# Kernel tuning notes

Measured on AMD Instinct MI355X. Metric: run time of the kernel, lower is better.

The kernel has to match this reference:

```python
import jax, jax.numpy as jnp
import numpy as np

N = 20000        # nodes
E = 640000       # edges (avg degree 32)
IN, H1, H2 = 512, 256, 128

def setup_inputs() -> dict:
    key = jax.random.key(0)
    k_feat, k_ew, k_src, k_dst, k_w1, k_w2 = jax.random.split(key, 6)
    return {
        "features": jax.random.normal(k_feat, (N, IN), jnp.float32),
        "edge_weight": jax.random.uniform(k_ew, (E,), jnp.float32),
        "src": jax.random.randint(k_src, (E,), 0, N),
        "dst": jax.random.randint(k_dst, (E,), 0, N),
        # learned params (GraphConv weight uses xavier-style init; bias zeros)
        "W1": jax.random.normal(k_w1, (IN, H1), jnp.float32) / np.float32(np.sqrt(IN)),
        "b1": jnp.zeros((H1,), jnp.float32),
        "W2": jax.random.normal(k_w2, (H1, H2), jnp.float32) / np.float32(np.sqrt(H1)),
        "b2": jnp.zeros((H2,), jnp.float32),
    }

def reference(features, edge_weight, src, dst, W1, b1, W2, b2):
    seg = lambda v, idx: jax.ops.segment_sum(v, idx, num_segments=N)

    # --- EdgeWeightNorm(norm='both'):
    # w_e / sqrt(out_wsum(src_e) * in_wsum(dst_e))
    out_wsum = seg(edge_weight, src)           # weighted out-degree  [N]
    in_wsum = seg(edge_weight, dst)            # weighted in-degree   [N]
    nw = edge_weight * jax.lax.rsqrt(out_wsum[src]) * jax.lax.rsqrt(in_wsum[dst])  # [E]

    # --- GraphConv layer 1: norm='none', edge_weight=nw, relu
    # in_feats > out_feats -> transform first, then weighted aggregation
    h = features @ W1                          # [N, H1]
    h = seg(h[src] * nw[:, None], dst) + b1    # SpMM: sum_e nw_e * h[src_e] at dst
    h = jax.nn.relu(h)

    # --- GraphConv layer 2: norm='both' (plain degrees, clamped min 1), identity act
    ones_e = jnp.ones((E,), h.dtype)
    out_deg = jnp.maximum(seg(ones_e, src), 1.0)   # out-degrees [N]
    in_deg = jnp.maximum(seg(ones_e, dst), 1.0)    # in-degrees  [N]
    h = h * jax.lax.rsqrt(out_deg)[:, None]        # src-side norm
    h = h @ W2                                     # [N, H2] (in > out -> W first)
    h = seg(h[src], dst)                           # unweighted sum aggregation
    h = h * jax.lax.rsqrt(in_deg)[:, None] + b2    # dst-side norm + bias
    return h
```

## Files before the change

kernel.cpp:

```cpp
#include <hip/hip_runtime.h>
#include <hip/hip_bf16.h>
#include <hip/hip_fp16.h>
#include <stdint.h>

#define IN_F 512
#define H1_F 256
#define H2_F 128
#define MPAD 20096
#define NN   20000
#define NPAIR 10000
#define BH   128
#define CAP  128
#define GB1  (157 * 2)

typedef __attribute__((ext_vector_type(8))) _Float16 half8;
typedef __attribute__((ext_vector_type(4))) float f32x4;
typedef __attribute__((ext_vector_type(4))) uint32_t u32x4;

__device__ inline __half2 h2cast(uint32_t v) { return __builtin_bit_cast(__half2, v); }
__device__ inline uint32_t h2bits(__half2 v) { return __builtin_bit_cast(uint32_t, v); }

__device__ inline void gld_lds16(const uint32_t* g, uint32_t* l) {
    __builtin_amdgcn_global_load_lds((const __attribute__((address_space(1))) uint32_t*)g,
                                     (__attribute__((address_space(3))) uint32_t*)l,
                                     16, 0, 0);
}

__global__ __launch_bounds__(512) void build_and_pack(
        const int* __restrict__ dst, const int* __restrict__ src,
        const float* __restrict__ ew,
        uint32_t* __restrict__ Pd, uint32_t* __restrict__ Ps, int E, int CH,
        const float4* __restrict__ X, ushort4* __restrict__ P, int n4,
        const float* __restrict__ W1, const float* __restrict__ W2,
        uint16_t* __restrict__ Bt1, uint16_t* __restrict__ Bt2) {
    __shared__ uint32_t pd[NN];
    __shared__ uint32_t ps[NN];
    const int b = blockIdx.x, tid = threadIdx.x;
    if (b < BH) {
        for (int i = tid; i < NN; i += 512) { pd[i] = 0; ps[i] = 0; }
        __syncthreads();
        const int e0 = b * CH, e1 = min(e0 + CH, E);
        for (int e = e0 + tid; e < e1; e += 512) {
            uint32_t v = (1u << 24) | (uint32_t)__float2uint_rn(ew[e] * 65536.0f);
            atomicAdd(&pd[dst[e]], v);
            atomicAdd(&ps[src[e]], v);
        }
        __syncthreads();
        for (int i = tid; i < NN; i += 512) {
            Pd[(size_t)b * NN + i] = pd[i];
            Ps[(size_t)b * NN + i] = ps[i];
        }
    } else {
        const int pbid = b - BH;
        const int PBLK = gridDim.x - BH;
        const int stride = PBLK * 512;
        const int t1 = IN_F * H1_F;
        const int total = n4 + t1 + H1_F * H2_F;
        for (int idx = pbid * 512 + tid; idx < total; idx += stride) {
            if (idx < n4) {
                float4 x = X[idx];
                ushort4 o;
                o.x = __builtin_bit_cast(unsigned short, (_Float16)x.x);
                o.y = __builtin_bit_cast(unsigned short, (_Float16)x.y);
                o.z = __builtin_bit_cast(unsigned short, (_Float16)x.z);
                o.w = __builtin_bit_cast(unsigned short, (_Float16)x.w);
                P[idx] = o;
            } else {
                int i = idx - n4;
                if (i < t1) {
                    int k = i / H1_F, n = i - k * H1_F;
                    Bt1[(size_t)n * IN_F + k] =
                        __builtin_bit_cast(unsigned short, (_Float16)W1[i]);
                } else {
                    int i2 = i - t1;
                    int k = i2 / H2_F, n = i2 - k * H2_F;
                    Bt2[(size_t)n * H1_F + k] =
                        __builtin_bit_cast(unsigned short, (_Float16)W2[i2]);
                }
            }
        }
    }
}

__global__ __launch_bounds__(256, 1) void gemm1_and_offsets(
        const uint16_t* __restrict__ At, const uint16_t* __restrict__ Bt,
        __half* __restrict__ Cout, int M, int K,
        const uint32_t* __restrict__ Pd, const uint32_t* __restrict__ Ps,
        uint16_t* __restrict__ Od,
        int* __restrict__ in_cnt, int* __restrict__ out_cnt,
        float* __restrict__ in_rs, float* __restrict__ out_rs, int N) {
    __shared__ uint32_t Al[128 * 16];
    __shared__ uint32_t Bl[128 * 16];
    const int bx = blockIdx.x;
    const int tid = threadIdx.x;
    if (bx >= GB1) {
        int i = (bx - GB1) * 256 + tid;
        if (i >= N) return;
        uint32_t cin = 0, cout = 0, win = 0, wout = 0;
        for (int b = 0; b < BH; ++b) {
            uint32_t vd = Pd[(size_t)b * NN + i];
            Od[(size_t)b * NN + i] = (uint16_t)cin;
            cin += vd >> 24; win += vd & 0xFFFFFFu;
            uint32_t vs = Ps[(size_t)b * NN + i];
            cout += vs >> 24; wout += vs & 0xFFFFFFu;
        }
        in_cnt[i] = (int)cin;
        out_cnt[i] = (int)cout;
        in_rs[i]  = cin  ? rsqrtf((float)win  * (1.0f / 65536.0f)) : 0.f;
        out_rs[i] = cout ? rsqrtf((float)wout * (1.0f / 65536.0f)) : 0.f;
        return;
    }
    const int xg = bx % 157, yg = bx / 157;
    const int lane = tid & 63, wid = tid >> 6;
    const int wm = wid >> 1, wn = wid & 1;
    const int l15 = lane & 15, lhi = lane >> 4;
    const int brow = xg * 128, bcol = yg * 128;

    f32x4 acc[4][4];
#pragma unroll
    for (int m = 0; m < 4; ++m)
#pragma unroll
        for (int n = 0; n < 4; ++n) acc[m][n] = f32x4{0.f, 0.f, 0.f, 0.f};

    for (int k0 = 0; k0 < K; k0 += 32) {
#pragma unroll
        for (int i = 0; i < 2; ++i) {
            int chunk = i * 256 + tid;
            int r = chunk >> 2, c16 = chunk & 3;
            int c16s = c16 ^ ((r & 3) ^ ((r >> 2) & 3));
            gld_lds16((const uint32_t*)(At + (size_t)(brow + r) * K + k0) + c16s * 4,
                      Al + chunk * 4);
        }
#pragma unroll
        for (int i = 0; i < 2; ++i) {
            int chunk = i * 256 + tid;
            int r = chunk >> 2, c16 = chunk & 3;
            int c16s = c16 ^ ((r & 3) ^ ((r >> 2) & 3));
            gld_lds16((const uint32_t*)(Bt + (size_t)(bcol + r) * K + k0) + c16s * 4,
                      Bl + chunk * 4);
        }
        __syncthreads();

        half8 am[4], bm[4];
#pragma unroll
        for (int m = 0; m < 4; ++m) {
            int row = wm * 64 + m * 16 + l15;
            int sA = (row & 3) ^ ((row >> 2) & 3);
            am[m] = __builtin_bit_cast(half8,
                        *(const u32x4*)(Al + row * 16 + ((lhi ^ sA) << 2)));
        }
#pragma unroll
        for (int n = 0; n < 4; ++n) {
            int col = wn * 64 + n * 16 + l15;
            int sB = (col & 3) ^ ((col >> 2) & 3);
            bm[n] = __builtin_bit_cast(half8,
                        *(const u32x4*)(Bl + col * 16 + ((lhi ^ sB) << 2)));
        }

#pragma unroll
        for (int m = 0; m < 4; ++m)
#pragma unroll
            for (int n = 0; n < 4; ++n)
                acc[m][n] = __builtin_amdgcn_mfma_f32_16x16x32_f16(am[m], bm[n],
                                                                   acc[m][n], 0, 0, 0);
        __syncthreads();
    }

#pragma unroll
    for (int m = 0; m < 4; ++m) {
        int rbase = brow + wm * 64 + m * 16 + lhi * 4;
#pragma unroll
        for (int n = 0; n < 4; ++n) {
            int col = bcol + wn * 64 + n * 16 + l15;
#pragma unroll
            for (int j = 0; j < 4; ++j) {
                int row = rbase + j;
                if (row < M)
                    Cout[(size_t)row * H1_F + col] = __float2half(acc[m][n][j]);
            }
        }
    }
}

__global__ __launch_bounds__(512) void scatter_dst(
        const int* __restrict__ src, const int* __restrict__ dst,
        const float* __restrict__ ew,
        const uint16_t* __restrict__ Od,
        const float* __restrict__ in_rs, const float* __restrict__ out_rs,
        unsigned long long* __restrict__ s_pk, int E, int CH) {
    __shared__ uint32_t h[NPAIR];
    const int b = blockIdx.x, tid = threadIdx.x;
    for (int i = tid; i < NPAIR; i += 512) h[i] = 0;
    __syncthreads();
    const int e0 = b * CH, e1 = min(e0 + CH, E);
    const uint16_t* Ob = Od + (size_t)b * NN;
    for (int e = e0 + tid; e < e1; e += 512) {
        int d = dst[e];
        uint32_t old = atomicAdd(&h[d >> 1], 1u << ((d & 1) * 16));
        uint32_t rank = (old >> ((d & 1) * 16)) & 0xffffu;
        int s = src[e];
        float nw = ew[e] * out_rs[s] * in_rs[d];
        int p = d * CAP + (int)Ob[d] + (int)rank;
        s_pk[p] = (unsigned long long)(unsigned)s |
                  ((unsigned long long)__builtin_bit_cast(unsigned, nw) << 32);
    }
}

__global__ __launch_bounds__(256, 1) void gemm2_f16(
        const uint16_t* __restrict__ At, const uint16_t* __restrict__ Bt,
        __half* __restrict__ Cout, const int* __restrict__ rowcnt,
        int M, int Nout, int K) {
    __shared__ uint32_t Al[128 * 16];
    __shared__ uint32_t Bl[128 * 16];
    const int tid = threadIdx.x;
    const int lane = tid & 63, wid = tid >> 6;
    const int wm = wid >> 1, wn = wid & 1;
    const int l15 = lane & 15, lhi = lane >> 4;
    const int brow = blockIdx.x * 128, bcol = blockIdx.y * 128;

    f32x4 acc[4][4];
#pragma unroll
    for (int m = 0; m < 4; ++m)
#pragma unroll
        for (int n = 0; n < 4; ++n) acc[m][n] = f32x4{0.f, 0.f, 0.f, 0.f};

    for (int k0 = 0; k0 < K; k0 += 32) {
#pragma unroll
        for (int i = 0; i < 2; ++i) {
            int chunk = i * 256 + tid;
            int r = chunk >> 2, c16 = chunk & 3;
            int c16s = c16 ^ ((r & 3) ^ ((r >> 2) & 3));
            gld_lds16((const uint32_t*)(At + (size_t)(brow + r) * K + k0) + c16s * 4,
                      Al + chunk * 4);
        }
#pragma unroll
        for (int i = 0; i < 2; ++i) {
            int chunk = i * 256 + tid;
            int r = chunk >> 2, c16 = chunk & 3;
            int c16s = c16 ^ ((r & 3) ^ ((r >> 2) & 3));
            gld_lds16((const uint32_t*)(Bt + (size_t)(bcol + r) * K + k0) + c16s * 4,
                      Bl + chunk * 4);
        }
        __syncthreads();

        half8 am[4], bm[4];
#pragma unroll
        for (int m = 0; m < 4; ++m) {
            int row = wm * 64 + m * 16 + l15;
            int sA = (row & 3) ^ ((row >> 2) & 3);
            am[m] = __builtin_bit_cast(half8,
                        *(const u32x4*)(Al + row * 16 + ((lhi ^ sA) << 2)));
        }
#pragma unroll
        for (int n = 0; n < 4; ++n) {
            int col = wn * 64 + n * 16 + l15;
            int sB = (col & 3) ^ ((col >> 2) & 3);
            bm[n] = __builtin_bit_cast(half8,
                        *(const u32x4*)(Bl + col * 16 + ((lhi ^ sB) << 2)));
        }

#pragma unroll
        for (int m = 0; m < 4; ++m)
#pragma unroll
            for (int n = 0; n < 4; ++n)
                acc[m][n] = __builtin_amdgcn_mfma_f32_16x16x32_f16(am[m], bm[n],
                                                                   acc[m][n], 0, 0, 0);
        __syncthreads();
    }

#pragma unroll
    for (int m = 0; m < 4; ++m) {
        int rbase = brow + wm * 64 + m * 16 + lhi * 4;
        float scl[4];
#pragma unroll
        for (int j = 0; j < 4; ++j) {
            scl[j] = 1.f;
            if (rbase + j < M)
                scl[j] = rsqrtf(fmaxf((float)rowcnt[rbase + j], 1.f));
        }
#pragma unroll
        for (int n = 0; n < 4; ++n) {
            int col = bcol + wn * 64 + n * 16 + l15;
#pragma unroll
            for (int j = 0; j < 4; ++j) {
                int row = rbase + j;
                if (row < M)
                    Cout[(size_t)row * Nout + col] = __float2half(acc[m][n][j] * scl[j]);
            }
        }
    }
}

__global__ void spmm1_h2(const uint4* __restrict__ h4,
                         const unsigned long long* __restrict__ s_pk,
                         const int* __restrict__ in_cnt,
                         const float* __restrict__ b1, uint16_t* __restrict__ h1f, int N) {
    int bx = blockIdx.x;
    int slice = bx & 3;
    int grp = bx >> 2;
    int wid = threadIdx.x >> 6, lane = threadIdx.x & 63;
    int node = grp * 4 + wid;
    if (node >= N) return;
    int start = node * CAP, cnt = in_cnt[node];
    int s_pre = 0; uint32_t w2_pre = 0;
    if (lane < cnt) {
        unsigned long long m = s_pk[start + lane];
        s_pre = (int)(unsigned)m;
        __half hw = __float2half(__builtin_bit_cast(float, (unsigned)(m >> 32)));
        w2_pre = h2bits(__halves2half2(hw, hw));
    }
    int el = lane >> 3, fo = lane & 7;
    const uint4* hb = h4 + slice * 8 + fo;
    __half2 acc[4];
#pragma unroll
    for (int k = 0; k < 4; ++k) acc[k] = h2cast(0u);
    int cnt1 = min(cnt, 64);
    int nb = (cnt1 + 7) >> 3;
    int s[8]; uint32_t w[8]; uint4 v[8];
#pragma unroll
    for (int g = 0; g < 8; ++g) {
        if (g < nb) {
            int j = el + g * 8;
            s[g] = __shfl(s_pre, j);
            w[g] = (uint32_t)__shfl((int)w2_pre, j);
            v[g] = hb[(size_t)s[g] * 32];
        }
    }
#pragma unroll
    for (int g = 0; g < 8; ++g) {
        if (g < nb) {
            __half2 wg = h2cast(w[g]);
            acc[0] = __hfma2(wg, h2cast(v[g].x), acc[0]);
            acc[1] = __hfma2(wg, h2cast(v[g].y), acc[1]);
            acc[2] = __hfma2(wg, h2cast(v[g].z), acc[2]);
            acc[3] = __hfma2(wg, h2cast(v[g].w), acc[3]);
        }
    }
    for (int j = 64 + el; j < cnt; j += 8) {
        unsigned long long m = s_pk[start + j];
        int sx = (int)(unsigned)m;
        __half hw = __float2half(__builtin_bit_cast(float, (unsigned)(m >> 32)));
        __half2 w2h = __halves2half2(hw, hw);
        uint4 vx = hb[(size_t)sx * 32];
        acc[0] = __hfma2(w2h, h2cast(vx.x), acc[0]);
        acc[1] = __hfma2(w2h, h2cast(vx.y), acc[1]);
        acc[2] = __hfma2(w2h, h2cast(vx.z), acc[2]);
        acc[3] = __hfma2(w2h, h2cast(vx.w), acc[3]);
    }
#pragma unroll
    for (int d = 8; d < 64; d <<= 1)
#pragma unroll
        for (int k = 0; k < 4; ++k) {
            uint32_t o = (uint32_t)__shfl_xor((int)h2bits(acc[k]), d);
            acc[k] = __hadd2(acc[k], h2cast(o));
        }
    if (el == 0) {
        int fi = slice * 64 + fo * 8;
        float2 f0 = __half22float2(acc[0]);
        float2 f1 = __half22float2(acc[1]);
        float2 f2 = __half22float2(acc[2]);
        float2 f3 = __half22float2(acc[3]);
        uint4 o;
        o.x = h2bits(__halves2half2(__float2half(fmaxf(f0.x + b1[fi + 0], 0.f)),
                                    __float2half(fmaxf(f0.y + b1[fi + 1], 0.f))));
        o.y = h2bits(__halves2half2(__float2half(fmaxf(f1.x + b1[fi + 2], 0.f)),
                                    __float2half(fmaxf(f1.y + b1[fi + 3], 0.f))));
        o.z = h2bits(__halves2half2(__float2half(fmaxf(f2.x + b1[fi + 4], 0.f)),
                                    __float2half(fmaxf(f2.y + b1[fi + 5], 0.f))));
        o.w = h2bits(__halves2half2(__float2half(fmaxf(f3.x + b1[fi + 6], 0.f)),
                                    __float2half(fmaxf(f3.y + b1[fi + 7], 0.f))));
        *(uint4*)(h1f + (size_t)node * H1_F + fi) = o;
    }
}

__global__ void spmm2_h2(const uint4* __restrict__ h4,
                         const unsigned long long* __restrict__ s_pk,
                         const int* __restrict__ in_cnt,
                         const float* __restrict__ b2, float* __restrict__ out, int N) {
    const uint32_t ONE2 = 0x3C003C00u;
    int bx = blockIdx.x;
    int slice = bx & 1;
    int grp = bx >> 1;
    int wid = threadIdx.x >> 6, lane = threadIdx.x & 63;
    int node = grp * 4 + wid;
    if (node >= N) return;
    int start = node * CAP, cnt = in_cnt[node];
    int s_pre = 0;
    if (lane < cnt) s_pre = (int)(unsigned)s_pk[start + lane];
    int el = lane >> 3, fo = lane & 7;
    const uint4* hb = h4 + slice * 8 + fo;
    __half2 acc0[4], acc1[4];
#pragma unroll
    for (int k = 0; k < 4; ++k) { acc0[k] = h2cast(0u); acc1[k] = h2cast(0u); }
    int cnt1 = min(cnt, 64);
    int nb = (cnt1 + 7) >> 3;
    int s[8]; __half2 w[8]; uint4 v[8];
#pragma unroll
    for (int g = 0; g < 8; ++g) {
        if (g < nb) {
            int j = el + g * 8;
            s[g] = __shfl(s_pre, j);
            w[g] = h2cast((j < cnt1) ? ONE2 : 0u);
            v[g] = hb[(size_t)s[g] * 16];
        }
    }
#pragma unroll
    for (int g = 0; g < 4; ++g) {
        if (g < nb) {
            acc0[0] = __hfma2(w[g], h2cast(v[g].x), acc0[0]);
            acc0[1] = __hfma2(w[g], h2cast(v[g].y), acc0[1]);
            acc0[2] = __hfma2(w[g], h2cast(v[g].z), acc0[2]);
            acc0[3] = __hfma2(w[g], h2cast(v[g].w), acc0[3]);
        }
    }
#pragma unroll
    for (int g = 4; g < 8; ++g) {
        if (g < nb) {
            acc1[0] = __hfma2(w[g], h2cast(v[g].x), acc1[0]);
            acc1[1] = __hfma2(w[g], h2cast(v[g].y), acc1[1]);
            acc1[2] = __hfma2(w[g], h2cast(v[g].z), acc1[2]);
            acc1[3] = __hfma2(w[g], h2cast(v[g].w), acc1[3]);
        }
    }
    for (int j = 64 + el; j < cnt; j += 8) {
        int sx = (int)(unsigned)s_pk[start + j];
        uint4 vx = hb[(size_t)sx * 16];
        __half2 one = h2cast(ONE2);
        acc0[0] = __hfma2(one, h2cast(vx.x), acc0[0]);
        acc0[1] = __hfma2(one, h2cast(vx.y), acc0[1]);
        acc0[2] = __hfma2(one, h2cast(vx.z), acc0[2]);
        acc0[3] = __hfma2(one, h2cast(vx.w), acc0[3]);
    }
    float accf[8];
#pragma unroll
    for (int k = 0; k < 4; ++k) {
        float2 a = __half22float2(acc0[k]);
        float2 b = __half22float2(acc1[k]);
        accf[2 * k]     = a.x + b.x;
        accf[2 * k + 1] = a.y + b.y;
    }
#pragma unroll
    for (int d = 8; d < 64; d <<= 1)
#pragma unroll
        for (int k = 0; k < 8; ++k) accf[k] += __shfl_xor(accf[k], d);
    if (el == 0) {
        float rin = rsqrtf(fmaxf((float)cnt, 1.f));
        int fi = slice * 64 + fo * 8;
        f32x4 r0, r1;
        r0.x = accf[0] * rin + b2[fi + 0];
        r0.y = accf[1] * rin + b2[fi + 1];
        r0.z = accf[2] * rin + b2[fi + 2];
        r0.w = accf[3] * rin + b2[fi + 3];
        r1.x = accf[4] * rin + b2[fi + 4];
        r1.y = accf[5] * rin + b2[fi + 5];
        r1.z = accf[6] * rin + b2[fi + 6];
        r1.w = accf[7] * rin + b2[fi + 7];
        float* dp = out + (size_t)node * H2_F + fi;
        *(f32x4*)dp = r0;
        *(f32x4*)(dp + 4) = r1;
    }
}

extern "C" void kernel_launch(void* const* d_in, const int* in_sizes, int n_in,
                              void* d_out, int out_size, void* d_ws, size_t ws_size,
                              hipStream_t stream) {
    const float* features = (const float*)d_in[0];
    const float* edge_w   = (const float*)d_in[1];
    const int*   src      = (const int*)d_in[2];
    const int*   dst      = (const int*)d_in[3];
    const float* W1       = (const float*)d_in[4];
    const float* b1       = (const float*)d_in[5];
    const float* W2       = (const float*)d_in[6];
    const float* b2       = (const float*)d_in[7];
    float* out = (float*)d_out;

    const int N = in_sizes[0] / IN_F;
    const int E = in_sizes[1];
    const int CH = (E + BH - 1) / BH;

    char* base = (char*)d_ws;
    size_t off = 0;
    auto alloc = [&](size_t bytes) {
        char* p = base + off;
        off = (off + bytes + 255) & ~(size_t)255;
        return p;
    };
    int*   out_cnt   = (int*)  alloc((size_t)N * 4);
    float* out_rs    = (float*)alloc((size_t)N * 4);
    int*   in_cnt    = (int*)  alloc((size_t)N * 4);
    float* in_rs     = (float*)alloc((size_t)N * 4);
    unsigned long long* s_pk = (unsigned long long*)alloc((size_t)NN * CAP * 8);
    uint16_t* Bt1    = (uint16_t*)alloc((size_t)H1_F * IN_F * 2);
    uint16_t* Bt2    = (uint16_t*)alloc((size_t)H2_F * H1_F * 2);
    __half* h_f16    = (__half*)alloc((size_t)MPAD * H1_F * 2);
    uint16_t* feat16 = (uint16_t*)alloc((size_t)MPAD * IN_F * 2);
    uint32_t* big    = (uint32_t*)alloc((size_t)BH * NN * 4 * 2 + (size_t)BH * NN * 2);
    uint32_t* Pd = big;
    uint32_t* Ps = big + (size_t)BH * NN;
    uint16_t* Od = (uint16_t*)(Ps + (size_t)BH * NN);
    uint16_t* h1f = (uint16_t*)big;
    __half*   h2f = (__half*)((uint16_t*)big + (size_t)MPAD * H1_F);
    (void)ws_size;

    build_and_pack<<<256, 512, 0, stream>>>(dst, src, edge_w, Pd, Ps, E, CH,
                                            (const float4*)features, (ushort4*)feat16,
                                            N * IN_F / 4, W1, W2, Bt1, Bt2);

    int goBlocks = GB1 + (N + 255) / 256;
    gemm1_and_offsets<<<goBlocks, 256, 0, stream>>>(feat16, Bt1, h_f16, N, IN_F,
                                                    Pd, Ps, Od, in_cnt, out_cnt,
                                                    in_rs, out_rs, N);

    scatter_dst<<<BH, 512, 0, stream>>>(src, dst, edge_w, Od,
                                        in_rs, out_rs, s_pk, E, CH);

    int grp = (N + 3) / 4;
    spmm1_h2<<<grp * 4, 256, 0, stream>>>((const uint4*)h_f16, s_pk,
                                          in_cnt, b1, h1f, N);
    dim3 g2(MPAD / 128, 1);
    gemm2_f16<<<g2, 256, 0, stream>>>(h1f, Bt2, h2f, out_cnt, N, H2_F, H1_F);
    spmm2_h2<<<grp * 2, 256, 0, stream>>>((const uint4*)h2f, s_pk,
                                          in_cnt, b2, out, N);
}
```

Before: 127.7 us.

## Fuse fp32-to-fp16 feature conversion into GEMM1 A-tile loads

The separate pass that converted the feature matrix to fp16 inside build_and_pack is removed. GEMM1 now reads fp32 features directly, converts them to fp16 in registers, and writes the swizzled tile to LDS, with row indices clamped to M-1. This drops a full write and re-read of the fp16 feature buffer, but GEMM1 now reads twice the bytes per A tile and replaces the asynchronous global-to-LDS loads with synchronous register loads.

```diff
diff --git a/kernel.cpp b/kernel.cpp
--- a/kernel.cpp
+++ b/kernel.cpp
@@ -26,11 +26,15 @@
                                      16, 0, 0);
 }
 
+__device__ inline uint32_t packh2(float a, float b) {
+    return (uint32_t)__builtin_bit_cast(unsigned short, (_Float16)a) |
+           ((uint32_t)__builtin_bit_cast(unsigned short, (_Float16)b) << 16);
+}
+
 __global__ __launch_bounds__(512) void build_and_pack(
         const int* __restrict__ dst, const int* __restrict__ src,
         const float* __restrict__ ew,
         uint32_t* __restrict__ Pd, uint32_t* __restrict__ Ps, int E, int CH,
-        const float4* __restrict__ X, ushort4* __restrict__ P, int n4,
         const float* __restrict__ W1, const float* __restrict__ W2,
         uint16_t* __restrict__ Bt1, uint16_t* __restrict__ Bt2) {
     __shared__ uint32_t pd[NN];
@@ -55,35 +59,24 @@
         const int PBLK = gridDim.x - BH;
         const int stride = PBLK * 512;
         const int t1 = IN_F * H1_F;
-        const int total = n4 + t1 + H1_F * H2_F;
-        for (int idx = pbid * 512 + tid; idx < total; idx += stride) {
-            if (idx < n4) {
-                float4 x = X[idx];
-                ushort4 o;
-                o.x = __builtin_bit_cast(unsigned short, (_Float16)x.x);
-                o.y = __builtin_bit_cast(unsigned short, (_Float16)x.y);
-                o.z = __builtin_bit_cast(unsigned short, (_Float16)x.z);
-                o.w = __builtin_bit_cast(unsigned short, (_Float16)x.w);
-                P[idx] = o;
+        const int total = t1 + H1_F * H2_F;
+        for (int i = pbid * 512 + tid; i < total; i += stride) {
+            if (i < t1) {
+                int k = i / H1_F, n = i - k * H1_F;
+                Bt1[(size_t)n * IN_F + k] =
+                    __builtin_bit_cast(unsigned short, (_Float16)W1[i]);
             } else {
-                int i = idx - n4;
-                if (i < t1) {
-                    int k = i / H1_F, n = i - k * H1_F;
-                    Bt1[(size_t)n * IN_F + k] =
-                        __builtin_bit_cast(unsigned short, (_Float16)W1[i]);
-                } else {
-                    int i2 = i - t1;
-                    int k = i2 / H2_F, n = i2 - k * H2_F;
-                    Bt2[(size_t)n * H1_F + k] =
-                        __builtin_bit_cast(unsigned short, (_Float16)W2[i2]);
-                }
+                int i2 = i - t1;
+                int k = i2 / H2_F, n = i2 - k * H2_F;
+                Bt2[(size_t)n * H1_F + k] =
+                    __builtin_bit_cast(unsigned short, (_Float16)W2[i2]);
             }
         }
     }
 }
 
 __global__ __launch_bounds__(256, 1) void gemm1_and_offsets(
-        const uint16_t* __restrict__ At, const uint16_t* __restrict__ Bt,
+        const float* __restrict__ A, const uint16_t* __restrict__ Bt,
         __half* __restrict__ Cout, int M, int K,
         const uint32_t* __restrict__ Pd, const uint32_t* __restrict__ Ps,
         uint16_t* __restrict__ Od,
@@ -125,11 +118,20 @@
     for (int k0 = 0; k0 < K; k0 += 32) {
 #pragma unroll
         for (int i = 0; i < 2; ++i) {
-            int chunk = i * 256 + tid;
-            int r = chunk >> 2, c16 = chunk & 3;
-            int c16s = c16 ^ ((r & 3) ^ ((r >> 2) & 3));
-            gld_lds16((const uint32_t*)(At + (size_t)(brow + r) * K + k0) + c16s * 4,
-                      Al + chunk * 4);
+            int g = i * 256 + tid;
+            int r = g >> 2, c16 = g & 3;
+            int sA = (r & 3) ^ ((r >> 2) & 3);
+            int c16s = c16 ^ sA;
+            int gr = min(brow + r, M - 1);
+            const float* gp = A + (size_t)gr * K + k0 + c16s * 8;
+            float4 fa = *(const float4*)gp;
+            float4 fb = *(const float4*)(gp + 4);
+            u32x4 q;
+            q.x = packh2(fa.x, fa.y);
+            q.y = packh2(fa.z, fa.w);
+            q.z = packh2(fb.x, fb.y);
+            q.w = packh2(fb.z, fb.w);
+            *(u32x4*)(Al + g * 4) = q;
         }
 #pragma unroll
         for (int i = 0; i < 2; ++i) {
@@ -493,7 +495,6 @@
     uint16_t* Bt1    = (uint16_t*)alloc((size_t)H1_F * IN_F * 2);
     uint16_t* Bt2    = (uint16_t*)alloc((size_t)H2_F * H1_F * 2);
     __half* h_f16    = (__half*)alloc((size_t)MPAD * H1_F * 2);
-    uint16_t* feat16 = (uint16_t*)alloc((size_t)MPAD * IN_F * 2);
     uint32_t* big    = (uint32_t*)alloc((size_t)BH * NN * 4 * 2 + (size_t)BH * NN * 2);
     uint32_t* Pd = big;
     uint32_t* Ps = big + (size_t)BH * NN;
@@ -503,11 +504,10 @@
     (void)ws_size;
 
     build_and_pack<<<256, 512, 0, stream>>>(dst, src, edge_w, Pd, Ps, E, CH,
-                                            (const float4*)features, (ushort4*)feat16,
-                                            N * IN_F / 4, W1, W2, Bt1, Bt2);
+                                            W1, W2, Bt1, Bt2);
 
     int goBlocks = GB1 + (N + 255) / 256;
-    gemm1_and_offsets<<<goBlocks, 256, 0, stream>>>(feat16, Bt1, h_f16, N, IN_F,
+    gemm1_and_offsets<<<goBlocks, 256, 0, stream>>>(features, Bt1, h_f16, N, IN_F,
                                                     Pd, Ps, Od, in_cnt, out_cnt,
                                                     in_rs, out_rs, N);
 
```

After: 122.7 us (median of 2 runs). 3.9% less time.
